# Optimization experiments

Measured on AMD Instinct MI355X. Metric: run time of the kernel, lower is better.

Reference implementation:

```python
import jax, jax.numpy as jnp
import numpy as np

# Module config (matches init_kwargs)
H, W = 512, 512          # in_dims
KH, KW = 32, 32          # kernel_dims
SH, SW = 16, 16          # stride
PH, PW = 8, 8            # padding
B = 64                   # batch
FULL_H, FULL_W = H + 2 * PH, W + 2 * PW            # 528, 528
NKH = 1 + (FULL_H - KH) // SH                      # 32
NKW = 1 + (FULL_W - KW) // SW                      # 32
NK = NKH * NKW                                     # 1024 output positions


def _patch_indices() -> np.ndarray:
    """Flat indices into the padded image for each sliding window.

    Reproduces the connectivity matrix columns of _create_connectivity_matrix:
    window k starts at (row*SH)*FULL_W + col*SW. Returns (NK, KH*KW) int32.
    """
    dr, dc = np.meshgrid(np.arange(KH), np.arange(KW), indexing="ij")
    off = (dr * FULL_W + dc).reshape(-1)                       # (KH*KW,)
    starts = (np.arange(NKH)[:, None] * SH * FULL_W
              + np.arange(NKW)[None, :] * SW).reshape(-1)      # (NK,)
    return (starts[:, None] + off[None, :]).astype(np.int32)


_IDX = jnp.asarray(_patch_indices())  # (NK, KH*KW), constant layout


def setup_inputs() -> dict:
    key = jax.random.key(0)
    kx, kw, kb = jax.random.split(key, 3)
    x = jax.random.normal(kx, (B, 1, H, W), dtype=jnp.float32)
    # Per-window weights = BSR values of the masked dense (padded_total, NK) matrix.
    # Xavier-normal scale of the underlying dense linear.
    std = float(np.sqrt(2.0 / (FULL_H * FULL_W + NK)))
    weight = jax.random.normal(kw, (NK, KH * KW), dtype=jnp.float32) * std
    bias = jax.random.normal(kb, (NK,), dtype=jnp.float32) * 0.01
    return {"x": x, "weight": weight, "bias": bias}


def reference(x, weight, bias):
    # x: (B, 1, H, W) -> pad -> flatten to (B, FULL_H*FULL_W)
    xp = jnp.pad(x, ((0, 0), (0, 0), (PH, PH), (PW, PW)))
    xf = xp.reshape(x.shape[0], FULL_H * FULL_W)
    # Gather the KHxKW window for every output position: (B, NK, KH*KW).
    patches = jnp.take(xf, _IDX, axis=1)
    # Untied locally-connected contraction (the block-sparse GEMM) + bias.
    out = jnp.einsum("bnk,nk->bn", patches, weight) + bias
    return out.reshape(x.shape[0], NKH, NKW)
```

## Files before the change

### kernel.cpp

```cpp
#include <hip/hip_runtime.h>

#define IMG_H 512
#define IMG_W 512
#define NKH 32
#define NKW 32
#define NK (NKH * NKW)
#define BATCH 64
#define NT 33

__global__ __launch_bounds__(256)
void bslc_tile_kernel(const float* __restrict__ x,
                      const float* __restrict__ w,
                      float* __restrict__ partial)
{
    __shared__ float4 xt[64][64];
    const int tc = blockIdx.x;
    const int tr = blockIdx.y;
    const int t  = threadIdx.x;
    const int lane = t & 63;
    const int wv   = t >> 6;

    const int kc = lane;
    const int r  = kc >> 2;
    const int c4 = kc & 3;
    const int rimg = tr * 16 - 8 + r;
    const int cimg = tc * 16 - 8 + c4 * 4;
    const bool interior = (tr >= 1) & (tr <= 31) & (tc >= 1) & (tc <= 31);
    const size_t xoff = (size_t)rimg * IMG_W + cimg;
    const int col = (0 + kc) & 63;

    if (interior) {
#pragma unroll
        for (int i = 0; i < 16; ++i) {
            const int b = wv + 4 * i;
            const float4 xv = *reinterpret_cast<const float4*>(
                x + (size_t)b * (IMG_H * IMG_W) + xoff);
            xt[kc][(b + kc) & 63] = xv;
        }
    } else {
#pragma unroll
        for (int i = 0; i < 16; ++i) {
            const int b = wv + 4 * i;
            float4 xv = make_float4(0.f, 0.f, 0.f, 0.f);
            if (rimg >= 0 && rimg < IMG_H) {
                const float* xb = x + (size_t)b * (IMG_H * IMG_W)
                                + (size_t)rimg * IMG_W;
#pragma unroll
                for (int e = 0; e < 4; ++e) {
                    const int c = cimg + e;
                    if (c >= 0 && c < IMG_W) (&xv.x)[e] = xb[c];
                }
            }
            xt[kc][(b + kc) & 63] = xv;
        }
    }
    (void)col;
    __syncthreads();

    const int q  = __builtin_amdgcn_readfirstlane(wv);
    const int qr = q >> 1, qc = q & 1;
    const int nr = tr - qr, nc = tc - qc;
    if (nr >= 0 && nr < NKH && nc >= 0 && nc < NKW) {
        const int n = nr * NKW + nc;
        const float* wq = w + (size_t)n * 1024 + (size_t)(qr * 16) * 32 + qc * 16;
        const int b = lane;

        float s0 = 0.f, s1 = 0.f, s2 = 0.f, s3 = 0.f;
#pragma unroll
        for (int kk = 0; kk < 64; ++kk) {
            const float4 xv = xt[kk][(b + kk) & 63];
            const float4 wv4 = *reinterpret_cast<const float4*>(
                wq + (kk >> 2) * 32 + (kk & 3) * 4);
            s0 = fmaf(xv.x, wv4.x, s0);
            s1 = fmaf(xv.y, wv4.y, s1);
            s2 = fmaf(xv.z, wv4.z, s2);
            s3 = fmaf(xv.w, wv4.w, s3);
        }
        partial[((size_t)q * NK + n) * 64 + b] = (s0 + s1) + (s2 + s3);
    }
}

__global__ __launch_bounds__(256)
void bslc_reduce_kernel(const float* __restrict__ partial,
                        const float* __restrict__ bias,
                        float* __restrict__ out)
{
    const int g = blockIdx.x * 256 + threadIdx.x;
    const int n = g >> 6;
    const int b = g & 63;
    float s = bias[n];
#pragma unroll
    for (int q = 0; q < 4; ++q)
        s += partial[((size_t)q * NK + n) * 64 + b];
    out[(size_t)b * NK + n] = s;
}

extern "C" void kernel_launch(void* const* d_in, const int* in_sizes, int n_in,
                              void* d_out, int out_size, void* d_ws, size_t ws_size,
                              hipStream_t stream) {
    const float* x    = (const float*)d_in[0];
    const float* wgt  = (const float*)d_in[1];
    const float* bias = (const float*)d_in[2];
    float* out        = (float*)d_out;
    float* partial    = (float*)d_ws;

    dim3 grid1(NT, NT);
    bslc_tile_kernel<<<grid1, 256, 0, stream>>>(x, wgt, partial);

    dim3 grid2((BATCH * NK) / 256);
    bslc_reduce_kernel<<<grid2, 256, 0, stream>>>(partial, bias, out);
}
```

Baseline: 122.3 us.

## Restructure into row-strip kernel with register-resident weights and pre-transformed weight layout

Replaces the 33x33 tile grid with one block per 16-row image strip and per pair of batch images. A new pre-pass kernel re-lays out the weights so each thread holds its 32 float4 weights in registers, reused across the batch images in the block. Each strip loads full image rows into skewed shared memory, and partial sums are reduced within quads by shuffles. A slimmer reduce kernel combines the top and bottom half-window contributions. This adds a third launch and a weight re-layout pass each call, and raises register pressure.

Result: slower. 156.6 us (+28.0%).

```diff
diff --git a/kernel.cpp b/kernel.cpp
--- a/kernel.cpp
+++ b/kernel.cpp
@@ -6,93 +6,127 @@
 #define NKW 32
 #define NK (NKH * NKW)
 #define BATCH 64
-#define NT 33
+#define NSTRIP 33
+#define G 2
 
 __global__ __launch_bounds__(256)
-void bslc_tile_kernel(const float* __restrict__ x,
-                      const float* __restrict__ w,
-                      float* __restrict__ partial)
+void bslc_wxform_kernel(const float* __restrict__ w, float4* __restrict__ W2)
 {
-    __shared__ float4 xt[64][64];
-    const int tc = blockIdx.x;
-    const int tr = blockIdx.y;
+    const int idx = blockIdx.x * 256 + threadIdx.x;
+    const int t    = idx & 255;
+    const int e    = (idx >> 8) & 7;
+    const int rr   = (idx >> 11) & 3;
+    const int tr   = idx >> 13;
+
+    const int h    = t >> 7;
+    const int nc   = (t >> 2) & 31;
+    const int rsub = t & 3;
+    const int nr   = tr - h;
+
+    float4 v = make_float4(0.f, 0.f, 0.f, 0.f);
+    const int ic0 = 16 * nc - 8 + 4 * e;
+    if (nr >= 0 && nr < NKH && ic0 >= 0 && ic0 < IMG_W) {
+        const int n = nr * NKW + nc;
+        const size_t off = (size_t)n * 1024 + (size_t)h * 512
+                         + (size_t)(rsub + 4 * rr) * 32 + 4 * e;
+        v = *reinterpret_cast<const float4*>(w + off);
+    }
+    W2[idx] = v;
+}
+
+__global__ __launch_bounds__(256, 4)
+void bslc_strip_kernel(const float* __restrict__ x,
+                       const float4* __restrict__ W2,
+                       float* __restrict__ P)
+{
+    __shared__ float4 xs[16 * 128];
+    const int tr = blockIdx.x;
+    const int bg = blockIdx.y;
     const int t  = threadIdx.x;
-    const int lane = t & 63;
-    const int wv   = t >> 6;
 
-    const int kc = lane;
-    const int r  = kc >> 2;
-    const int c4 = kc & 3;
-    const int rimg = tr * 16 - 8 + r;
-    const int cimg = tc * 16 - 8 + c4 * 4;
-    const bool interior = (tr >= 1) & (tr <= 31) & (tc >= 1) & (tc <= 31);
-    const size_t xoff = (size_t)rimg * IMG_W + cimg;
-    const int col = (0 + kc) & 63;
+    const int h    = t >> 7;
+    const int nc   = (t >> 2) & 31;
+    const int rsub = t & 3;
 
-    if (interior) {
+    float4 wreg[4][8];
+    {
+        const float4* wt = W2 + (size_t)tr * 8192 + t;
 #pragma unroll
-        for (int i = 0; i < 16; ++i) {
-            const int b = wv + 4 * i;
-            const float4 xv = *reinterpret_cast<const float4*>(
-                x + (size_t)b * (IMG_H * IMG_W) + xoff);
-            xt[kc][(b + kc) & 63] = xv;
+        for (int rr = 0; rr < 4; ++rr)
+#pragma unroll
+            for (int e = 0; e < 8; ++e)
+                wreg[rr][e] = wt[(rr * 8 + e) * 256];
+    }
+
+    const int r0img = tr * 16 - 8;
+    const bool interior = (tr >= 1) && (tr <= 31);
+
+    for (int bi = 0; bi < G; ++bi) {
+        const int b = bg * G + bi;
+        const float* xb = x + (size_t)b * (IMG_H * IMG_W);
+
+        if (interior) {
+            const float4* src = reinterpret_cast<const float4*>(
+                xb + (size_t)r0img * IMG_W);
+#pragma unroll
+            for (int i = 0; i < 8; ++i) {
+                const int g  = i * 256 + t;
+                const int r  = g >> 7;
+                const int c  = g & 127;
+                xs[r * 128 + ((c + r) & 127)] = src[g];
+            }
+        } else {
+#pragma unroll
+            for (int i = 0; i < 8; ++i) {
+                const int g  = i * 256 + t;
+                const int r  = g >> 7;
+                const int c  = g & 127;
+                const int rimg = r0img + r;
+                float4 v = make_float4(0.f, 0.f, 0.f, 0.f);
+                if (rimg >= 0 && rimg < IMG_H)
+                    v = *reinterpret_cast<const float4*>(
+                        xb + (size_t)rimg * IMG_W + 4 * c);
+                xs[r * 128 + ((c + r) & 127)] = v;
+            }
         }
-    } else {
+        __syncthreads();
+
+        float a0 = 0.f, a1 = 0.f, a2 = 0.f, a3 = 0.f;
 #pragma unroll
-        for (int i = 0; i < 16; ++i) {
-            const int b = wv + 4 * i;
-            float4 xv = make_float4(0.f, 0.f, 0.f, 0.f);
-            if (rimg >= 0 && rimg < IMG_H) {
-                const float* xb = x + (size_t)b * (IMG_H * IMG_W)
-                                + (size_t)rimg * IMG_W;
+        for (int rr = 0; rr < 4; ++rr) {
+            const int r = rsub + 4 * rr;
+            const int cbase = 4 * nc - 2 + r;
 #pragma unroll
-                for (int e = 0; e < 4; ++e) {
-                    const int c = cimg + e;
-                    if (c >= 0 && c < IMG_W) (&xv.x)[e] = xb[c];
-                }
+            for (int e = 0; e < 8; ++e) {
+                const float4 xv = xs[r * 128 + ((cbase + e) & 127)];
+                const float4 wv = wreg[rr][e];
+                a0 = fmaf(xv.x, wv.x, a0);
+                a1 = fmaf(xv.y, wv.y, a1);
+                a2 = fmaf(xv.z, wv.z, a2);
+                a3 = fmaf(xv.w, wv.w, a3);
             }
-            xt[kc][(b + kc) & 63] = xv;
         }
-    }
-    (void)col;
-    __syncthreads();
-
-    const int q  = __builtin_amdgcn_readfirstlane(wv);
-    const int qr = q >> 1, qc = q & 1;
-    const int nr = tr - qr, nc = tc - qc;
-    if (nr >= 0 && nr < NKH && nc >= 0 && nc < NKW) {
-        const int n = nr * NKW + nc;
-        const float* wq = w + (size_t)n * 1024 + (size_t)(qr * 16) * 32 + qc * 16;
-        const int b = lane;
-
-        float s0 = 0.f, s1 = 0.f, s2 = 0.f, s3 = 0.f;
-#pragma unroll
-        for (int kk = 0; kk < 64; ++kk) {
-            const float4 xv = xt[kk][(b + kk) & 63];
-            const float4 wv4 = *reinterpret_cast<const float4*>(
-                wq + (kk >> 2) * 32 + (kk & 3) * 4);
-            s0 = fmaf(xv.x, wv4.x, s0);
-            s1 = fmaf(xv.y, wv4.y, s1);
-            s2 = fmaf(xv.z, wv4.z, s2);
-            s3 = fmaf(xv.w, wv4.w, s3);
-        }
-        partial[((size_t)q * NK + n) * 64 + b] = (s0 + s1) + (s2 + s3);
+        float s = (a0 + a1) + (a2 + a3);
+        s += __shfl_xor(s, 1, 64);
+        s += __shfl_xor(s, 2, 64);
+        if (rsub == 0)
+            P[((size_t)b * NSTRIP + tr) * 64 + h * 32 + nc] = s;
+        __syncthreads();
     }
 }
 
 __global__ __launch_bounds__(256)
-void bslc_reduce_kernel(const float* __restrict__ partial,
+void bslc_reduce_kernel(const float* __restrict__ P,
                         const float* __restrict__ bias,
                         float* __restrict__ out)
 {
     const int g = blockIdx.x * 256 + threadIdx.x;
-    const int n = g >> 6;
-    const int b = g & 63;
-    float s = bias[n];
-#pragma unroll
-    for (int q = 0; q < 4; ++q)
-        s += partial[((size_t)q * NK + n) * 64 + b];
-    out[(size_t)b * NK + n] = s;
+    const int b = g >> 10;
+    const int n = g & (NK - 1);
+    const int nr = n >> 5, nc = n & 31;
+    const float top = P[((size_t)b * NSTRIP + nr) * 64 + nc];
+    const float bot = P[((size_t)b * NSTRIP + nr + 1) * 64 + 32 + nc];
+    out[g] = top + bot + bias[n];
 }
 
 extern "C" void kernel_launch(void* const* d_in, const int* in_sizes, int n_in,
@@ -102,11 +136,11 @@
     const float* wgt  = (const float*)d_in[1];
     const float* bias = (const float*)d_in[2];
     float* out        = (float*)d_out;
-    float* partial    = (float*)d_ws;
 
-    dim3 grid1(NT, NT);
-    bslc_tile_kernel<<<grid1, 256, 0, stream>>>(x, wgt, partial);
+    float*  P  = (float*)d_ws;
+    float4* W2 = (float4*)((char*)d_ws + 64 * NSTRIP * 64 * sizeof(float));
 
-    dim3 grid2((BATCH * NK) / 256);
-    bslc_reduce_kernel<<<grid2, 256, 0, stream>>>(partial, bias, out);
+    bslc_wxform_kernel<<<dim3(NSTRIP * 8192 / 256), 256, 0, stream>>>(wgt, W2);
+    bslc_strip_kernel<<<dim3(NSTRIP, BATCH / G), 256, 0, stream>>>(x, W2, P);
+    bslc_reduce_kernel<<<dim3(BATCH * NK / 256), 256, 0, stream>>>(P, bias, out);
 }
```

## Split batch across two blocks per tile with XCD-aware remapping and wave-split reduction

Applied to the files above, without the earlier changes.

Each 16x16 input tile is now handled by two blocks, each covering half the batch. This halves shared memory per block and doubles the grid. Block IDs are remapped so neighbouring tiles land on the same XCD, which should improve L2 reuse of overlapping weights and inputs. Inside a wave the 64 k-chunks are split across two half-waves and combined with a cross-lane shuffle. The edge-tile loads are simplified to whole-float4 validity checks, and the partial-sum layout is reindexed by tile, so the reduce kernel computes tile indices to gather its four contributions.

After: 108.7 us. 11.1% less time.

```diff
diff --git a/kernel.cpp b/kernel.cpp
--- a/kernel.cpp
+++ b/kernel.cpp
@@ -4,94 +4,103 @@
 #define IMG_W 512
 #define NKH 32
 #define NKW 32
-#define NK (NKH * NKW)
+#define NK 1024
 #define BATCH 64
-#define NT 33
+#define NTT 33
+#define NTILE (NTT * NTT)
+#define NBLK (NTILE * 2)
 
-__global__ __launch_bounds__(256)
-void bslc_tile_kernel(const float* __restrict__ x,
-                      const float* __restrict__ w,
-                      float* __restrict__ partial)
+__global__ __launch_bounds__(256, 4)
+void bslc_main(const float* __restrict__ x,
+               const float* __restrict__ w,
+               float* __restrict__ P)
 {
-    __shared__ float4 xt[64][64];
-    const int tc = blockIdx.x;
-    const int tr = blockIdx.y;
-    const int t  = threadIdx.x;
-    const int lane = t & 63;
-    const int wv   = t >> 6;
+    __shared__ float4 xt[64][32];
 
-    const int kc = lane;
-    const int r  = kc >> 2;
-    const int c4 = kc & 3;
-    const int rimg = tr * 16 - 8 + r;
-    const int cimg = tc * 16 - 8 + c4 * 4;
+    const int hw   = blockIdx.x;
+    const int xcd  = hw & 7, slot = hw >> 3;
+    const int q8   = NBLK >> 3, r8 = NBLK & 7;
+    const int work = (xcd < r8 ? xcd * (q8 + 1)
+                               : r8 * (q8 + 1) + (xcd - r8) * q8) + slot;
+
+    const int bg  = work & 1;
+    const int lin = work >> 1;
+    const int tr  = lin / NTT, tc = lin % NTT;
+
+    const int t = threadIdx.x, lane = t & 63, wv = t >> 6;
+
+    const int r0 = tr * 16 - 8, c0 = tc * 16 - 8;
+    const int kk = lane;
+    const int rimg = r0 + (kk >> 2);
+    const int cimg = c0 + (kk & 3) * 4;
     const bool interior = (tr >= 1) & (tr <= 31) & (tc >= 1) & (tc <= 31);
     const size_t xoff = (size_t)rimg * IMG_W + cimg;
-    const int col = (0 + kc) & 63;
 
     if (interior) {
 #pragma unroll
-        for (int i = 0; i < 16; ++i) {
-            const int b = wv + 4 * i;
-            const float4 xv = *reinterpret_cast<const float4*>(
-                x + (size_t)b * (IMG_H * IMG_W) + xoff);
-            xt[kc][(b + kc) & 63] = xv;
+        for (int i = 0; i < 8; ++i) {
+            const int b = i * 4 + wv;
+            const float4 v = *reinterpret_cast<const float4*>(
+                x + (size_t)(bg * 32 + b) * (IMG_H * IMG_W) + xoff);
+            xt[kk][(b + kk) & 31] = v;
         }
     } else {
+        const bool ok = (rimg >= 0) & (rimg < IMG_H) & (cimg >= 0) & (cimg < IMG_W);
 #pragma unroll
-        for (int i = 0; i < 16; ++i) {
-            const int b = wv + 4 * i;
-            float4 xv = make_float4(0.f, 0.f, 0.f, 0.f);
-            if (rimg >= 0 && rimg < IMG_H) {
-                const float* xb = x + (size_t)b * (IMG_H * IMG_W)
-                                + (size_t)rimg * IMG_W;
-#pragma unroll
-                for (int e = 0; e < 4; ++e) {
-                    const int c = cimg + e;
-                    if (c >= 0 && c < IMG_W) (&xv.x)[e] = xb[c];
-                }
-            }
-            xt[kc][(b + kc) & 63] = xv;
+        for (int i = 0; i < 8; ++i) {
+            const int b = i * 4 + wv;
+            float4 v = make_float4(0.f, 0.f, 0.f, 0.f);
+            if (ok)
+                v = *reinterpret_cast<const float4*>(
+                    x + (size_t)(bg * 32 + b) * (IMG_H * IMG_W) + xoff);
+            xt[kk][(b + kk) & 31] = v;
         }
     }
-    (void)col;
     __syncthreads();
 
-    const int q  = __builtin_amdgcn_readfirstlane(wv);
-    const int qr = q >> 1, qc = q & 1;
+    const int qr = wv >> 1, qc = wv & 1;
     const int nr = tr - qr, nc = tc - qc;
-    if (nr >= 0 && nr < NKH && nc >= 0 && nc < NKW) {
-        const int n = nr * NKW + nc;
-        const float* wq = w + (size_t)n * 1024 + (size_t)(qr * 16) * 32 + qc * 16;
-        const int b = lane;
+    if (nr < 0 || nr >= NKH || nc < 0 || nc >= NKW) return;
 
-        float s0 = 0.f, s1 = 0.f, s2 = 0.f, s3 = 0.f;
+    const int n    = nr * NKW + nc;
+    const int half = lane >> 5;
+    const int b    = lane & 31;
+    const float* wb = w + (size_t)n * 1024
+                    + (size_t)(qr * 16 + half * 8) * 32 + qc * 16;
+
+    float a0 = 0.f, a1 = 0.f, a2 = 0.f, a3 = 0.f;
 #pragma unroll
-        for (int kk = 0; kk < 64; ++kk) {
-            const float4 xv = xt[kk][(b + kk) & 63];
-            const float4 wv4 = *reinterpret_cast<const float4*>(
-                wq + (kk >> 2) * 32 + (kk & 3) * 4);
-            s0 = fmaf(xv.x, wv4.x, s0);
-            s1 = fmaf(xv.y, wv4.y, s1);
-            s2 = fmaf(xv.z, wv4.z, s2);
-            s3 = fmaf(xv.w, wv4.w, s3);
-        }
-        partial[((size_t)q * NK + n) * 64 + b] = (s0 + s1) + (s2 + s3);
+    for (int j = 0; j < 32; ++j) {
+        const int kq = half * 32 + j;
+        const float4 xv  = xt[kq][(b + kq) & 31];
+        const float4 wv4 = *reinterpret_cast<const float4*>(
+            wb + (j >> 2) * 32 + (j & 3) * 4);
+        a0 = fmaf(xv.x, wv4.x, a0);
+        a1 = fmaf(xv.y, wv4.y, a1);
+        a2 = fmaf(xv.z, wv4.z, a2);
+        a3 = fmaf(xv.w, wv4.w, a3);
     }
+    float s = (a0 + a1) + (a2 + a3);
+    s += __shfl_xor(s, 32, 64);
+    if (half == 0)
+        P[((size_t)(tr * NTT + tc) * 4 + wv) * 64 + bg * 32 + b] = s;
 }
 
 __global__ __launch_bounds__(256)
-void bslc_reduce_kernel(const float* __restrict__ partial,
-                        const float* __restrict__ bias,
-                        float* __restrict__ out)
+void bslc_reduce(const float* __restrict__ P,
+                 const float* __restrict__ bias,
+                 float* __restrict__ out)
 {
     const int g = blockIdx.x * 256 + threadIdx.x;
     const int n = g >> 6;
     const int b = g & 63;
+    const int nr = n >> 5, nc = n & 31;
     float s = bias[n];
 #pragma unroll
-    for (int q = 0; q < 4; ++q)
-        s += partial[((size_t)q * NK + n) * 64 + b];
+    for (int qq = 0; qq < 4; ++qq) {
+        const int tile = (nr + (qq >> 1)) * NTT + nc + (qq & 1);
+        s += P[((size_t)tile * 4 + qq) * 64 + b];
+    }
     out[(size_t)b * NK + n] = s;
 }
 
@@ -102,11 +111,8 @@
     const float* wgt  = (const float*)d_in[1];
     const float* bias = (const float*)d_in[2];
     float* out        = (float*)d_out;
-    float* partial    = (float*)d_ws;
+    float* P          = (float*)d_ws;
 
-    dim3 grid1(NT, NT);
-    bslc_tile_kernel<<<grid1, 256, 0, stream>>>(x, wgt, partial);
-
-    dim3 grid2((BATCH * NK) / 256);
-    bslc_reduce_kernel<<<grid2, 256, 0, stream>>>(partial, bias, out);
+    bslc_main<<<dim3(NBLK), 256, 0, stream>>>(x, wgt, P);
+    bslc_reduce<<<dim3(BATCH * NK / 256), 256, 0, stream>>>(P, bias, out);
 }
```
